# Optimization experiments

Measured on AMD Instinct MI355X. Metric: run time of the kernel, lower is better.

## Reference

```python
import jax, jax.numpy as jnp
import numpy as np

NUM_BINS = 3
TAIL_BOUND = 1.0


def conv3x3(x, w, b):
    # x: [B,C,H,W], w: [O,I,3,3]
    y = jax.lax.conv_general_dilated(x, w, (1, 1), 'SAME',
                                     dimension_numbers=('NCHW', 'OIHW', 'NCHW'))
    return y + b[None, :, None, None]


def unconstrained_linear_spline(inputs, unnormalized_pdf, tail_bound=TAIL_BOUND):
    # inputs: [B,C,H,W]; unnormalized_pdf: [B,C,H,W,num_bins]
    num_bins = unnormalized_pdf.shape[-1]
    left = bottom = -tail_bound
    right = top = tail_bound
    inside = (inputs >= left) & (inputs <= right)

    x = (inputs - left) / (right - left)  # scale to [0,1]
    pdf = jax.nn.softmax(unnormalized_pdf, axis=-1)
    cdf = jnp.cumsum(pdf, axis=-1)
    cdf = cdf.at[..., -1].set(1.0)
    cdf = jnp.pad(cdf, [(0, 0)] * (cdf.ndim - 1) + [(1, 0)])  # [..., num_bins+1]

    pos = jnp.clip(x, 0.0, 1.0) * num_bins  # clip keeps bin idx valid for outside elems
    bin_idx = jnp.clip(jnp.floor(pos).astype(jnp.int32), 0, num_bins - 1)
    alpha = pos - bin_idx.astype(pos.dtype)

    input_pdfs = jnp.take_along_axis(pdf, bin_idx[..., None], axis=-1)[..., 0]
    out = jnp.take_along_axis(cdf, bin_idx[..., None], axis=-1)[..., 0] + alpha * input_pdfs
    out = jnp.clip(out, 0.0, 1.0)
    lad = jnp.log(input_pdfs) + jnp.log(jnp.asarray(num_bins, pos.dtype))

    out = out * (top - bottom) + bottom
    lad = lad - jnp.log(jnp.asarray(top - bottom, pos.dtype)) + jnp.log(jnp.asarray(right - left, pos.dtype))

    out = jnp.where(inside, out, inputs)       # identity tails
    lad = jnp.where(inside, lad, 0.0)
    return out, lad


def setup_inputs() -> dict:
    key = jax.random.key(0)
    ks = jax.random.split(key, 4)
    B, C, H, W = 32, 64, 64, 64
    hidden = 128
    c_half = C // 2
    c_out = c_half * NUM_BINS
    x = jax.random.normal(ks[0], (B, C, H, W), dtype=jnp.float32)
    objective = jnp.zeros((B,), dtype=jnp.float32)
    W1 = jax.random.normal(ks[1], (hidden, c_half, 3, 3), dtype=jnp.float32) * 0.05
    b1 = jnp.zeros((hidden,), dtype=jnp.float32)
    W2 = jax.random.normal(ks[2], (c_out, hidden, 3, 3), dtype=jnp.float32) * 0.05
    b2 = jnp.zeros((c_out,), dtype=jnp.float32)
    return {'x': x, 'objective': objective, 'W1': W1, 'b1': b1, 'W2': W2, 'b2': b2}


def reference(x, objective, W1, b1, W2, b2):
    identity_split, transform_split = jnp.split(x, 2, axis=1)
    h = jax.nn.relu(conv3x3(identity_split, W1, b1))
    transform_params = conv3x3(h, W2, b2)  # [B, C/2*num_bins, H, W]
    b, c, hh, ww = transform_split.shape
    transform_params = transform_params.reshape(b, c, NUM_BINS, hh, ww).transpose(0, 1, 3, 4, 2)
    transformed, logabsdet = unconstrained_linear_spline(transform_split, transform_params)
    output = jnp.concatenate([identity_split, transformed], axis=1)
    objective_out = objective + jnp.sum(logabsdet.reshape(b, -1), axis=1)
    return output, objective_out
```

## Files before the change

kernel.cpp:

```cpp
#include <hip/hip_runtime.h>

typedef __attribute__((ext_vector_type(8))) __bf16 bf16x8;
typedef __attribute__((ext_vector_type(4))) float f32x4;

__device__ __forceinline__ unsigned short f2bf(float f) {
    unsigned int u = __builtin_bit_cast(unsigned int, f);
    u = (u + 0x7FFFu + ((u >> 16) & 1u)) >> 16;
    return (unsigned short)u;
}

__global__ void __launch_bounds__(256) prep_w(const float* __restrict__ W1,
                                              const float* __restrict__ W2,
                                              unsigned short* __restrict__ Wt1,
                                              unsigned short* __restrict__ Wt2) {
    int tid = blockIdx.x * 256 + threadIdx.x;
    if (tid < 36864) {
        int tt = tid % 9, rem = tid / 9;
        int i = rem & 31, o = rem >> 5;
        Wt1[(tt * 128 + o) * 32 + i] = f2bf(W1[tid]);
    }
    if (tid < 110592) {
        int tt = tid % 9, rem = tid / 9;
        int i = rem & 127, o = rem >> 7;
        int kc = i >> 6, ii = i & 63;
        int khalf = ii >> 5, kgrp = (ii >> 3) & 3, j = ii & 7;
        int o_tile = o >> 4, lrow = o & 15;
        int s = kc * 9 + tt;
        Wt2[(size_t)s * 6144 +
            (size_t)(((o_tile * 2 + khalf) * 64 + kgrp * 16 + lrow) * 8 + j)] = f2bf(W2[tid]);
    }
}

__global__ void __launch_bounds__(256) conv1_fused(const float* __restrict__ x,
                                                   const float* __restrict__ obj,
                                                   const float* __restrict__ b1,
                                                   const unsigned short* __restrict__ Wt1,
                                                   unsigned short* __restrict__ hbuf,
                                                   float* __restrict__ out) {
    const int LW = 40;
    __shared__ unsigned short sx[6 * 66 * LW];
    int wg = blockIdx.x;
    int b = wg >> 4, h0 = (wg & 15) << 2;
    int t = threadIdx.x;

#pragma unroll
    for (int j = 0; j < 8; ++j) {
        int idx = j * 256 + t;
        int c = idx >> 6, row = (idx >> 4) & 3, w4 = idx & 15;
        size_t off = (((size_t)b * 64 + c) * 64 + (h0 + row)) * 16 + w4;
        reinterpret_cast<float4*>(out)[off] =
            reinterpret_cast<const float4*>(x)[off];
    }
    if (wg == 0 && t < 32) out[8388608 + t] = obj[t];

    if (t < 48) {
        int row = t >> 3, k = t & 7;
        int col = (k & 1) ? 65 : 0, c0 = (k >> 1) * 8;
        *reinterpret_cast<uint4*>(&sx[(row * 66 + col) * LW + c0]) = uint4{0, 0, 0, 0};
    }
    {
        int w = t & 63, c4 = t >> 6;
        const float* xb = x + (size_t)b * 262144;
#pragma unroll
        for (int row = 0; row < 6; ++row) {
            int gh = h0 - 1 + row;
            if (gh >= 0 && gh < 64) {
                const float* xr = xb + (size_t)gh * 64;
#pragma unroll
                for (int co = 0; co < 8; ++co) {
                    int c = co * 4 + c4;
                    sx[(row * 66 + w + 1) * LW + c] = f2bf(xr[(size_t)c * 4096 + w]);
                }
            } else {
#pragma unroll
                for (int co = 0; co < 8; ++co) {
                    int c = co * 4 + c4;
                    sx[(row * 66 + w + 1) * LW + c] = 0;
                }
            }
        }
    }
    __syncthreads();

    int wid = t >> 6, lane = t & 63;
    int lrow = lane & 15, kgrp = lane >> 4;

    bf16x8 afr[2][9];
#pragma unroll
    for (int m2 = 0; m2 < 2; ++m2) {
        int o = (wid * 2 + m2) * 16 + lrow;
#pragma unroll
        for (int tap = 0; tap < 9; ++tap)
            afr[m2][tap] = *reinterpret_cast<const bf16x8*>(
                Wt1 + (size_t)(tap * 128 + o) * 32 + kgrp * 8);
    }

    for (int nt = 0; nt < 16; ++nt) {
        int r = nt >> 2, ww = ((nt & 3) << 4) + lrow;
        f32x4 acc0 = {0.f, 0.f, 0.f, 0.f}, acc1 = {0.f, 0.f, 0.f, 0.f};
#pragma unroll
        for (int dh = 0; dh < 3; ++dh)
#pragma unroll
            for (int dw = 0; dw < 3; ++dw) {
                int tap = dh * 3 + dw;
                bf16x8 bfr = *reinterpret_cast<const bf16x8*>(
                    &sx[((r + dh) * 66 + ww + dw) * LW + kgrp * 8]);
                acc0 = __builtin_amdgcn_mfma_f32_16x16x32_bf16(afr[0][tap], bfr, acc0, 0, 0, 0);
                acc1 = __builtin_amdgcn_mfma_f32_16x16x32_bf16(afr[1][tap], bfr, acc1, 0, 0, 0);
            }
        int hh = h0 + r;
        size_t obase = (((size_t)b * 64 + hh) * 64 + ww) * 128;
#pragma unroll
        for (int m2 = 0; m2 < 2; ++m2) {
            f32x4 a = (m2 == 0) ? acc0 : acc1;
            int o0 = (wid * 2 + m2) * 16 + kgrp * 4;
            unsigned short r4[4];
#pragma unroll
            for (int j = 0; j < 4; ++j) {
                float v = a[j] + b1[o0 + j];
                r4[j] = f2bf(fmaxf(v, 0.f));
            }
            uint2 pk;
            pk.x = (unsigned)r4[0] | ((unsigned)r4[1] << 16);
            pk.y = (unsigned)r4[2] | ((unsigned)r4[3] << 16);
            *reinterpret_cast<uint2*>(hbuf + obase + o0) = pk;
        }
    }
}

__global__ void __launch_bounds__(512) conv2_spline(const unsigned short* __restrict__ hbuf,
                                                    const float* __restrict__ b2,
                                                    const unsigned short* __restrict__ Wt2,
                                                    const float* __restrict__ x,
                                                    float* __restrict__ out) {
    const int LWA = 72;
    __shared__ __align__(16) unsigned short sa[4 * 66 * LWA];
    __shared__ float red[8];
    float* pm = reinterpret_cast<float*>(sa);

    int raw = blockIdx.x;
    int wg = (raw & 7) * 128 + (raw >> 3);
    int b = wg >> 5, h0 = (wg & 31) << 1;
    int t = threadIdx.x;
    int wid = t >> 6, lane = t & 63;
    int lrow = lane & 15, kgrp = lane >> 4;
    int mgrp = wid >> 2, ngrp = wid & 3;
    int mb = mgrp * 3;

    f32x4 acc[3][2];
#pragma unroll
    for (int i = 0; i < 3; ++i)
#pragma unroll
        for (int j = 0; j < 2; ++j) acc[i][j] = f32x4{0.f, 0.f, 0.f, 0.f};

    const unsigned short* wfb = Wt2 + (size_t)lane * 8;

    for (int kc2 = 0; kc2 < 2; ++kc2) {
        if (kc2) __syncthreads();
#pragma unroll
        for (int j = 0; j < 4; ++j) {
            int idx = j * 512 + t;
            int row = idx >> 9, rem = idx & 511;
            int w = rem >> 3, c0 = (rem & 7) * 8;
            int gh = h0 - 1 + row;
            uint4 v = uint4{0, 0, 0, 0};
            if (gh >= 0 && gh < 64)
                v = *reinterpret_cast<const uint4*>(
                    hbuf + (((size_t)b * 64 + gh) * 64 + w) * 128 + kc2 * 64 + c0);
            *reinterpret_cast<uint4*>(&sa[(row * 66 + (w + 1)) * LWA + c0]) = v;
        }
        if (t < 64) {
            int row = t >> 4, k = t & 15;
            int col = (k & 1) ? 65 : 0, c0 = (k >> 1) * 8;
            *reinterpret_cast<uint4*>(&sa[(row * 66 + col) * LWA + c0]) = uint4{0, 0, 0, 0};
        }
        __syncthreads();

#pragma unroll
        for (int tap = 0; tap < 9; ++tap) {
            int s = kc2 * 9 + tap;
            const unsigned short* wsl = wfb + (size_t)s * 6144;
            int dh = tap / 3, dw = tap % 3;
            bf16x8 wfr[3][2];
#pragma unroll
            for (int mi = 0; mi < 3; ++mi) {
                int ot = mb + mi;
                wfr[mi][0] = *reinterpret_cast<const bf16x8*>(wsl + (size_t)(ot * 2 + 0) * 512);
                wfr[mi][1] = *reinterpret_cast<const bf16x8*>(wsl + (size_t)(ot * 2 + 1) * 512);
            }
#pragma unroll
            for (int ni = 0; ni < 2; ++ni) {
                int nt = ngrp * 2 + ni;
                int rr = nt >> 2, wcol = (nt & 3) * 16 + lrow;
                int base = ((rr + dh) * 66 + wcol + dw) * LWA;
                bf16x8 a0 = *reinterpret_cast<const bf16x8*>(&sa[base + kgrp * 8]);
                bf16x8 a1 = *reinterpret_cast<const bf16x8*>(&sa[base + 32 + kgrp * 8]);
#pragma unroll
                for (int mi = 0; mi < 3; ++mi) {
                    acc[mi][ni] = __builtin_amdgcn_mfma_f32_16x16x32_bf16(wfr[mi][0], a0, acc[mi][ni], 0, 0, 0);
                    acc[mi][ni] = __builtin_amdgcn_mfma_f32_16x16x32_bf16(wfr[mi][1], a1, acc[mi][ni], 0, 0, 0);
                }
            }
        }
    }

    float lad_acc = 0.f;
    for (int half = 0; half < 2; ++half) {
        __syncthreads();
        if ((ngrp >> 1) == half) {
#pragma unroll
            for (int mi = 0; mi < 3; ++mi) {
                int o0 = (mb + mi) * 16 + kgrp * 4;
                float bb0 = b2[o0], bb1 = b2[o0 + 1], bb2 = b2[o0 + 2], bb3 = b2[o0 + 3];
#pragma unroll
                for (int ni = 0; ni < 2; ++ni) {
                    int p = ((ngrp & 1) * 2 + ni) * 16 + lrow;
                    f32x4 v = acc[mi][ni];
                    pm[p * 101 + o0]     = v[0] + bb0;
                    pm[p * 101 + o0 + 1] = v[1] + bb1;
                    pm[p * 101 + o0 + 2] = v[2] + bb2;
                    pm[p * 101 + o0 + 3] = v[3] + bb3;
                }
            }
        }
        __syncthreads();
#pragma unroll 4
        for (int it = 0; it < 4; ++it) {
            int idx = it * 512 + t;
            int c = idx >> 6, p = idx & 63;
            int pb = p * 101 + 3 * c;
            float u0 = pm[pb];
            float u1 = pm[pb + 1];
            float u2 = pm[pb + 2];
            size_t gpos = (size_t)(b * 64 + 32 + c) * 4096 + (size_t)(h0 + half) * 64 + p;
            float xin = x[gpos];
            float mx = fmaxf(u0, fmaxf(u1, u2));
            float e0 = __expf(u0 - mx), e1 = __expf(u1 - mx), e2 = __expf(u2 - mx);
            float s = e0 + e1 + e2;
            float inv = 1.0f / s;
            float pos01 = fminf(fmaxf((xin + 1.f) * 0.5f, 0.f), 1.f) * 3.f;
            int bin = (int)pos01; bin = bin > 2 ? 2 : bin;
            float alpha = pos01 - (float)bin;
            float eb = (bin == 0) ? e0 : ((bin == 1) ? e1 : e2);
            float cb = (bin == 0) ? 0.f : ((bin == 1) ? e0 : (e0 + e1));
            float pk = eb * inv;
            float outv = cb * inv + alpha * pk;
            outv = fminf(fmaxf(outv, 0.f), 1.f) * 2.f - 1.f;
            float lad = __logf(pk) + 1.09861228866810969f;
            bool inside = (xin >= -1.f) && (xin <= 1.f);
            if (!inside) { outv = xin; lad = 0.f; }
            out[gpos] = outv;
            lad_acc += lad;
        }
    }
#pragma unroll
    for (int off = 32; off > 0; off >>= 1)
        lad_acc += __shfl_down(lad_acc, off, 64);
    if (lane == 0) red[wid] = lad_acc;
    __syncthreads();
    if (t == 0) {
        float s = 0.f;
#pragma unroll
        for (int i = 0; i < 8; ++i) s += red[i];
        atomicAdd(out + 8388608 + b, s);
    }
}

extern "C" void kernel_launch(void* const* d_in, const int* in_sizes, int n_in,
                              void* d_out, int out_size, void* d_ws, size_t ws_size,
                              hipStream_t stream) {
    const float* x   = (const float*)d_in[0];
    const float* obj = (const float*)d_in[1];
    const float* W1  = (const float*)d_in[2];
    const float* b1  = (const float*)d_in[3];
    const float* W2  = (const float*)d_in[4];
    const float* b2  = (const float*)d_in[5];
    float* out = (float*)d_out;
    char* ws = (char*)d_ws;

    unsigned short* hbuf = (unsigned short*)ws;
    unsigned short* Wt1  = (unsigned short*)(ws + 33554432);
    unsigned short* Wt2  = (unsigned short*)(ws + 33554432 + 73728);

    hipLaunchKernelGGL(prep_w,       dim3(432),  dim3(256), 0, stream, W1, W2, Wt1, Wt2);
    hipLaunchKernelGGL(conv1_fused,  dim3(512),  dim3(256), 0, stream, x, obj, b1, Wt1, hbuf, out);
    hipLaunchKernelGGL(conv2_spline, dim3(1024), dim3(512), 0, stream, hbuf, b2, Wt2, x, out);
}
```

Baseline: 71.41 us.

## Fuse conv1 into conv2 kernel, recomputing halo rows in shared memory

Merges the first convolution into the second-conv/spline kernel. Each block recomputes the hidden activations for its two output rows plus a one-row halo directly into shared memory, in two 64-channel chunks. This removes the 32MB bf16 hidden-buffer round trip through global memory and one kernel launch. In exchange it recomputes conv1 for the halo rows (about double the conv1 FLOPs), raises per-block shared memory use, and adds syncs inside the block. The objective copy moves into the weight-prep kernel, and Wt1 gets a fragment-friendly layout.

```diff
diff --git a/kernel.cpp b/kernel.cpp
--- a/kernel.cpp
+++ b/kernel.cpp
@@ -11,13 +11,17 @@
 
 __global__ void __launch_bounds__(256) prep_w(const float* __restrict__ W1,
                                               const float* __restrict__ W2,
+                                              const float* __restrict__ obj,
                                               unsigned short* __restrict__ Wt1,
-                                              unsigned short* __restrict__ Wt2) {
+                                              unsigned short* __restrict__ Wt2,
+                                              float* __restrict__ out) {
     int tid = blockIdx.x * 256 + threadIdx.x;
+    if (tid < 32) out[8388608 + tid] = obj[tid];
     if (tid < 36864) {
         int tt = tid % 9, rem = tid / 9;
         int i = rem & 31, o = rem >> 5;
-        Wt1[(tt * 128 + o) * 32 + i] = f2bf(W1[tid]);
+        int mt = o >> 4, lr = o & 15, kg = i >> 3, j = i & 7;
+        Wt1[(size_t)((tt * 8 + mt) * 64 + kg * 16 + lr) * 8 + j] = f2bf(W1[tid]);
     }
     if (tid < 110592) {
         int tt = tid % 9, rem = tid / 9;
@@ -31,112 +35,18 @@
     }
 }
 
-__global__ void __launch_bounds__(256) conv1_fused(const float* __restrict__ x,
-                                                   const float* __restrict__ obj,
-                                                   const float* __restrict__ b1,
-                                                   const unsigned short* __restrict__ Wt1,
-                                                   unsigned short* __restrict__ hbuf,
-                                                   float* __restrict__ out) {
-    const int LW = 40;
-    __shared__ unsigned short sx[6 * 66 * LW];
-    int wg = blockIdx.x;
-    int b = wg >> 4, h0 = (wg & 15) << 2;
-    int t = threadIdx.x;
-
-#pragma unroll
-    for (int j = 0; j < 8; ++j) {
-        int idx = j * 256 + t;
-        int c = idx >> 6, row = (idx >> 4) & 3, w4 = idx & 15;
-        size_t off = (((size_t)b * 64 + c) * 64 + (h0 + row)) * 16 + w4;
-        reinterpret_cast<float4*>(out)[off] =
-            reinterpret_cast<const float4*>(x)[off];
-    }
-    if (wg == 0 && t < 32) out[8388608 + t] = obj[t];
-
-    if (t < 48) {
-        int row = t >> 3, k = t & 7;
-        int col = (k & 1) ? 65 : 0, c0 = (k >> 1) * 8;
-        *reinterpret_cast<uint4*>(&sx[(row * 66 + col) * LW + c0]) = uint4{0, 0, 0, 0};
-    }
-    {
-        int w = t & 63, c4 = t >> 6;
-        const float* xb = x + (size_t)b * 262144;
-#pragma unroll
-        for (int row = 0; row < 6; ++row) {
-            int gh = h0 - 1 + row;
-            if (gh >= 0 && gh < 64) {
-                const float* xr = xb + (size_t)gh * 64;
-#pragma unroll
-                for (int co = 0; co < 8; ++co) {
-                    int c = co * 4 + c4;
-                    sx[(row * 66 + w + 1) * LW + c] = f2bf(xr[(size_t)c * 4096 + w]);
-                }
-            } else {
-#pragma unroll
-                for (int co = 0; co < 8; ++co) {
-                    int c = co * 4 + c4;
-                    sx[(row * 66 + w + 1) * LW + c] = 0;
-                }
-            }
-        }
-    }
-    __syncthreads();
-
-    int wid = t >> 6, lane = t & 63;
-    int lrow = lane & 15, kgrp = lane >> 4;
-
-    bf16x8 afr[2][9];
-#pragma unroll
-    for (int m2 = 0; m2 < 2; ++m2) {
-        int o = (wid * 2 + m2) * 16 + lrow;
-#pragma unroll
-        for (int tap = 0; tap < 9; ++tap)
-            afr[m2][tap] = *reinterpret_cast<const bf16x8*>(
-                Wt1 + (size_t)(tap * 128 + o) * 32 + kgrp * 8);
-    }
-
-    for (int nt = 0; nt < 16; ++nt) {
-        int r = nt >> 2, ww = ((nt & 3) << 4) + lrow;
-        f32x4 acc0 = {0.f, 0.f, 0.f, 0.f}, acc1 = {0.f, 0.f, 0.f, 0.f};
-#pragma unroll
-        for (int dh = 0; dh < 3; ++dh)
-#pragma unroll
-            for (int dw = 0; dw < 3; ++dw) {
-                int tap = dh * 3 + dw;
-                bf16x8 bfr = *reinterpret_cast<const bf16x8*>(
-                    &sx[((r + dh) * 66 + ww + dw) * LW + kgrp * 8]);
-                acc0 = __builtin_amdgcn_mfma_f32_16x16x32_bf16(afr[0][tap], bfr, acc0, 0, 0, 0);
-                acc1 = __builtin_amdgcn_mfma_f32_16x16x32_bf16(afr[1][tap], bfr, acc1, 0, 0, 0);
-            }
-        int hh = h0 + r;
-        size_t obase = (((size_t)b * 64 + hh) * 64 + ww) * 128;
-#pragma unroll
-        for (int m2 = 0; m2 < 2; ++m2) {
-            f32x4 a = (m2 == 0) ? acc0 : acc1;
-            int o0 = (wid * 2 + m2) * 16 + kgrp * 4;
-            unsigned short r4[4];
-#pragma unroll
-            for (int j = 0; j < 4; ++j) {
-                float v = a[j] + b1[o0 + j];
-                r4[j] = f2bf(fmaxf(v, 0.f));
-            }
-            uint2 pk;
-            pk.x = (unsigned)r4[0] | ((unsigned)r4[1] << 16);
-            pk.y = (unsigned)r4[2] | ((unsigned)r4[3] << 16);
-            *reinterpret_cast<uint2*>(hbuf + obase + o0) = pk;
-        }
-    }
-}
-
-__global__ void __launch_bounds__(512) conv2_spline(const unsigned short* __restrict__ hbuf,
-                                                    const float* __restrict__ b2,
-                                                    const unsigned short* __restrict__ Wt2,
-                                                    const float* __restrict__ x,
-                                                    float* __restrict__ out) {
+__global__ void __launch_bounds__(512) mega(const float* __restrict__ x,
+                                            const float* __restrict__ b1,
+                                            const float* __restrict__ b2,
+                                            const unsigned short* __restrict__ Wt1,
+                                            const unsigned short* __restrict__ Wt2,
+                                            float* __restrict__ out) {
+    const int LWX = 40;
     const int LWA = 72;
-    __shared__ __align__(16) unsigned short sa[4 * 66 * LWA];
+    __shared__ __align__(16) unsigned short sx[6 * 66 * LWX];
+    __shared__ __align__(16) unsigned short hb[4 * 66 * LWA];
     __shared__ float red[8];
-    float* pm = reinterpret_cast<float*>(sa);
+    float* pm = reinterpret_cast<float*>(sx);
 
     int raw = blockIdx.x;
     int wg = (raw & 7) * 128 + (raw >> 3);
@@ -144,78 +54,151 @@
     int t = threadIdx.x;
     int wid = t >> 6, lane = t & 63;
     int lrow = lane & 15, kgrp = lane >> 4;
-    int mgrp = wid >> 2, ngrp = wid & 3;
-    int mb = mgrp * 3;
-
-    f32x4 acc[3][2];
+    int mg = wid >> 2, ng = wid & 3;
+    int mb2 = mg * 3;
+
+#pragma unroll
+    for (int j = 0; j < 2; ++j) {
+        int idx = j * 512 + t;
+        int c = idx >> 5, row = (idx >> 4) & 1, w4 = idx & 15;
+        size_t off = (((size_t)b * 64 + c) * 64 + (h0 + row)) * 16 + w4;
+        reinterpret_cast<float4*>(out)[off] = reinterpret_cast<const float4*>(x)[off];
+    }
+
+    if (t < 48) {
+        int row = t >> 3, k = t & 7;
+        int col = (k & 1) ? 65 : 0, c0 = (k >> 1) * 8;
+        *reinterpret_cast<uint4*>(&sx[(row * 66 + col) * LWX + c0]) = uint4{0, 0, 0, 0};
+    }
+    {
+        int w = t & 63, c4 = (t >> 6) * 4;
+        const float* xb = x + (size_t)b * 262144;
+#pragma unroll
+        for (int row = 0; row < 6; ++row) {
+            int gh = h0 - 2 + row;
+            unsigned short* srow = &sx[(row * 66 + w + 1) * LWX];
+            if ((unsigned)gh < 64u) {
+                const float* xr = xb + (size_t)gh * 64;
+#pragma unroll
+                for (int cc = 0; cc < 2; ++cc) {
+                    int c = c4 + cc * 2;
+                    unsigned pk = (unsigned)f2bf(xr[(size_t)c * 4096 + w]) |
+                                  ((unsigned)f2bf(xr[(size_t)(c + 1) * 4096 + w]) << 16);
+                    *reinterpret_cast<unsigned*>(&srow[c]) = pk;
+                }
+            } else {
+                *reinterpret_cast<unsigned*>(&srow[c4]) = 0u;
+                *reinterpret_cast<unsigned*>(&srow[c4 + 2]) = 0u;
+            }
+        }
+    }
+    if (t < 64) {
+        int row = t >> 4, k = t & 15;
+        int col = (k & 1) ? 65 : 0, c0 = (k >> 1) * 8;
+        *reinterpret_cast<uint4*>(&hb[(row * 66 + col) * LWA + c0]) = uint4{0, 0, 0, 0};
+    }
+    __syncthreads();
+
+    const unsigned short* wfb1 = Wt1 + (size_t)lane * 8;
+    const unsigned short* wfb2 = Wt2 + (size_t)lane * 8;
+
+    f32x4 acc2[3][2];
 #pragma unroll
     for (int i = 0; i < 3; ++i)
 #pragma unroll
-        for (int j = 0; j < 2; ++j) acc[i][j] = f32x4{0.f, 0.f, 0.f, 0.f};
-
-    const unsigned short* wfb = Wt2 + (size_t)lane * 8;
+        for (int j = 0; j < 2; ++j) acc2[i][j] = f32x4{0.f, 0.f, 0.f, 0.f};
 
     for (int kc2 = 0; kc2 < 2; ++kc2) {
-        if (kc2) __syncthreads();
-#pragma unroll
-        for (int j = 0; j < 4; ++j) {
-            int idx = j * 512 + t;
-            int row = idx >> 9, rem = idx & 511;
-            int w = rem >> 3, c0 = (rem & 7) * 8;
-            int gh = h0 - 1 + row;
-            uint4 v = uint4{0, 0, 0, 0};
-            if (gh >= 0 && gh < 64)
-                v = *reinterpret_cast<const uint4*>(
-                    hbuf + (((size_t)b * 64 + gh) * 64 + w) * 128 + kc2 * 64 + c0);
-            *reinterpret_cast<uint4*>(&sa[(row * 66 + (w + 1)) * LWA + c0]) = v;
-        }
-        if (t < 64) {
-            int row = t >> 4, k = t & 15;
-            int col = (k & 1) ? 65 : 0, c0 = (k >> 1) * 8;
-            *reinterpret_cast<uint4*>(&sa[(row * 66 + col) * LWA + c0]) = uint4{0, 0, 0, 0};
+        f32x4 acc1[2][4];
+#pragma unroll
+        for (int i = 0; i < 2; ++i)
+#pragma unroll
+            for (int j = 0; j < 4; ++j) acc1[i][j] = f32x4{0.f, 0.f, 0.f, 0.f};
+#pragma unroll
+        for (int tap = 0; tap < 9; ++tap) {
+            int dh = tap / 3, dw = tap % 3;
+            bf16x8 wa[2];
+#pragma unroll
+            for (int mi = 0; mi < 2; ++mi) {
+                int mt = kc2 * 4 + mg * 2 + mi;
+                wa[mi] = *reinterpret_cast<const bf16x8*>(wfb1 + (size_t)(tap * 8 + mt) * 512);
+            }
+#pragma unroll
+            for (int ni = 0; ni < 4; ++ni) {
+                int nt = ng * 4 + ni;
+                int hrow = nt >> 2, wt2 = nt & 3;
+                bf16x8 bx = *reinterpret_cast<const bf16x8*>(
+                    &sx[((hrow + dh) * 66 + wt2 * 16 + lrow + dw) * LWX + kgrp * 8]);
+#pragma unroll
+                for (int mi = 0; mi < 2; ++mi)
+                    acc1[mi][ni] = __builtin_amdgcn_mfma_f32_16x16x32_bf16(wa[mi], bx, acc1[mi][ni], 0, 0, 0);
+            }
+        }
+#pragma unroll
+        for (int mi = 0; mi < 2; ++mi) {
+            int chc = (mg * 2 + mi) * 16 + kgrp * 4;
+            int och = kc2 * 64 + chc;
+            float bb0 = b1[och], bb1 = b1[och + 1], bb2 = b1[och + 2], bb3 = b1[och + 3];
+#pragma unroll
+            for (int ni = 0; ni < 4; ++ni) {
+                int nt = ng * 4 + ni;
+                int hrow = nt >> 2, wt2 = nt & 3;
+                bool valid = (unsigned)(h0 - 1 + hrow) < 64u;
+                f32x4 v = acc1[mi][ni];
+                unsigned short r0 = valid ? f2bf(fmaxf(v[0] + bb0, 0.f)) : (unsigned short)0;
+                unsigned short r1 = valid ? f2bf(fmaxf(v[1] + bb1, 0.f)) : (unsigned short)0;
+                unsigned short r2 = valid ? f2bf(fmaxf(v[2] + bb2, 0.f)) : (unsigned short)0;
+                unsigned short r3 = valid ? f2bf(fmaxf(v[3] + bb3, 0.f)) : (unsigned short)0;
+                uint2 pk;
+                pk.x = (unsigned)r0 | ((unsigned)r1 << 16);
+                pk.y = (unsigned)r2 | ((unsigned)r3 << 16);
+                *reinterpret_cast<uint2*>(
+                    &hb[(hrow * 66 + wt2 * 16 + lrow + 1) * LWA + chc]) = pk;
+            }
         }
         __syncthreads();
 
 #pragma unroll
         for (int tap = 0; tap < 9; ++tap) {
             int s = kc2 * 9 + tap;
-            const unsigned short* wsl = wfb + (size_t)s * 6144;
+            const unsigned short* wsl = wfb2 + (size_t)s * 6144;
             int dh = tap / 3, dw = tap % 3;
             bf16x8 wfr[3][2];
 #pragma unroll
             for (int mi = 0; mi < 3; ++mi) {
-                int ot = mb + mi;
+                int ot = mb2 + mi;
                 wfr[mi][0] = *reinterpret_cast<const bf16x8*>(wsl + (size_t)(ot * 2 + 0) * 512);
                 wfr[mi][1] = *reinterpret_cast<const bf16x8*>(wsl + (size_t)(ot * 2 + 1) * 512);
             }
 #pragma unroll
             for (int ni = 0; ni < 2; ++ni) {
-                int nt = ngrp * 2 + ni;
+                int nt = ng * 2 + ni;
                 int rr = nt >> 2, wcol = (nt & 3) * 16 + lrow;
                 int base = ((rr + dh) * 66 + wcol + dw) * LWA;
-                bf16x8 a0 = *reinterpret_cast<const bf16x8*>(&sa[base + kgrp * 8]);
-                bf16x8 a1 = *reinterpret_cast<const bf16x8*>(&sa[base + 32 + kgrp * 8]);
+                bf16x8 a0 = *reinterpret_cast<const bf16x8*>(&hb[base + kgrp * 8]);
+                bf16x8 a1 = *reinterpret_cast<const bf16x8*>(&hb[base + 32 + kgrp * 8]);
 #pragma unroll
                 for (int mi = 0; mi < 3; ++mi) {
-                    acc[mi][ni] = __builtin_amdgcn_mfma_f32_16x16x32_bf16(wfr[mi][0], a0, acc[mi][ni], 0, 0, 0);
-                    acc[mi][ni] = __builtin_amdgcn_mfma_f32_16x16x32_bf16(wfr[mi][1], a1, acc[mi][ni], 0, 0, 0);
+                    acc2[mi][ni] = __builtin_amdgcn_mfma_f32_16x16x32_bf16(wfr[mi][0], a0, acc2[mi][ni], 0, 0, 0);
+                    acc2[mi][ni] = __builtin_amdgcn_mfma_f32_16x16x32_bf16(wfr[mi][1], a1, acc2[mi][ni], 0, 0, 0);
                 }
             }
         }
+        __syncthreads();
     }
 
     float lad_acc = 0.f;
     for (int half = 0; half < 2; ++half) {
-        __syncthreads();
-        if ((ngrp >> 1) == half) {
+        if (half) __syncthreads();
+        if ((ng >> 1) == half) {
 #pragma unroll
             for (int mi = 0; mi < 3; ++mi) {
-                int o0 = (mb + mi) * 16 + kgrp * 4;
+                int o0 = (mb2 + mi) * 16 + kgrp * 4;
                 float bb0 = b2[o0], bb1 = b2[o0 + 1], bb2 = b2[o0 + 2], bb3 = b2[o0 + 3];
 #pragma unroll
                 for (int ni = 0; ni < 2; ++ni) {
-                    int p = ((ngrp & 1) * 2 + ni) * 16 + lrow;
-                    f32x4 v = acc[mi][ni];
+                    int p = ((ng & 1) * 2 + ni) * 16 + lrow;
+                    f32x4 v = acc2[mi][ni];
                     pm[p * 101 + o0]     = v[0] + bb0;
                     pm[p * 101 + o0 + 1] = v[1] + bb1;
                     pm[p * 101 + o0 + 2] = v[2] + bb2;
@@ -278,11 +261,9 @@
     float* out = (float*)d_out;
     char* ws = (char*)d_ws;
 
-    unsigned short* hbuf = (unsigned short*)ws;
-    unsigned short* Wt1  = (unsigned short*)(ws + 33554432);
-    unsigned short* Wt2  = (unsigned short*)(ws + 33554432 + 73728);
-
-    hipLaunchKernelGGL(prep_w,       dim3(432),  dim3(256), 0, stream, W1, W2, Wt1, Wt2);
-    hipLaunchKernelGGL(conv1_fused,  dim3(512),  dim3(256), 0, stream, x, obj, b1, Wt1, hbuf, out);
-    hipLaunchKernelGGL(conv2_spline, dim3(1024), dim3(512), 0, stream, hbuf, b2, Wt2, x, out);
-}
+    unsigned short* Wt1 = (unsigned short*)ws;
+    unsigned short* Wt2 = (unsigned short*)(ws + 73728);
+
+    hipLaunchKernelGGL(prep_w, dim3(432),  dim3(256), 0, stream, W1, W2, obj, Wt1, Wt2, out);
+    hipLaunchKernelGGL(mega,   dim3(1024), dim3(512), 0, stream, x, b1, b2, Wt1, Wt2, out);
+}
```

Result: slower. 88.71 us (+24.2%).
